# Performance work log

Hardware: AMD Instinct MI355X
Metric: run time of the kernel (lower is better)

Reference implementation:

```python
import jax, jax.numpy as jnp
import numpy as np

KERNEL_MUL = 2.0
KERNEL_NUM = 5


def setup_inputs() -> dict:
    key = jax.random.key(0)
    k1, k2 = jax.random.split(key)
    n, d = 4096, 256
    source = jax.random.normal(k1, (n, d), dtype=jnp.float32)
    target = jax.random.normal(k2, (n, d), dtype=jnp.float32) + 0.5  # slight domain shift
    return {"source": source, "target": target}


def _gaussian_kernel_sum(source, target):
    # total: (2n, d)
    total = jnp.concatenate([source, target], axis=0)
    n_samples = total.shape[0]
    # Pairwise squared L2 via x^2 + y^2 - 2xy (same math as the (2n,2n,d) broadcast)
    sq = jnp.sum(total * total, axis=1)  # (2n,)
    l2 = sq[:, None] + sq[None, :] - 2.0 * (total @ total.T)  # (2n, 2n)
    l2 = jnp.maximum(l2, 0.0)
    # bandwidth from detached distances (torch uses L2_distance.data)
    bandwidth = jax.lax.stop_gradient(jnp.sum(l2)) / (n_samples ** 2 - n_samples)
    bandwidth = bandwidth / (KERNEL_MUL ** (KERNEL_NUM // 2))
    # sum of multi-bandwidth RBF kernels
    kernels = jnp.zeros_like(l2)
    for i in range(KERNEL_NUM):
        kernels = kernels + jnp.exp(-l2 / (bandwidth * (KERNEL_MUL ** i)))
    return kernels


def reference(source, target):
    b = source.shape[0]
    kernels = _gaussian_kernel_sum(source, target)
    xx = jnp.mean(kernels[:b, :b])
    yy = jnp.mean(kernels[b:, b:])
    xy = jnp.mean(kernels[:b, b:])
    yx = jnp.mean(kernels[b:, :b])
    return xx + yy - xy - yx
```

## Files before the change

### kernel.cpp

```cpp
#include <hip/hip_runtime.h>

#define N_TOT 8192
#define NB    4096
#define DDIM  256
#define NTILE 64
#define NBLK  (NTILE * (NTILE + 1) / 2)

typedef __bf16 bf16x8 __attribute__((ext_vector_type(8)));
typedef float  f32x4  __attribute__((ext_vector_type(4)));

__device__ inline unsigned short f2bf_rne(float x) {
    unsigned int u = __float_as_uint(x);
    unsigned int r = (u + 0x7fffu + ((u >> 16) & 1u)) >> 16;
    return (unsigned short)r;
}

__device__ inline void gl2lds16(const unsigned short* g, unsigned short* l) {
    __builtin_amdgcn_global_load_lds(
        (const __attribute__((address_space(1))) unsigned int*)g,
        (__attribute__((address_space(3))) unsigned int*)l, 16, 0, 0);
}


__global__ void prep_rows(const float* __restrict__ src, const float* __restrict__ tgt,
                          float* __restrict__ sq, unsigned short* __restrict__ totb) {
    int wid  = threadIdx.x >> 6;
    int lane = threadIdx.x & 63;
    int row  = blockIdx.x * 4 + wid;
    const float* rp = (row < NB) ? (src + (size_t)row * DDIM)
                                 : (tgt + (size_t)(row - NB) * DDIM);
    float4 v = ((const float4*)rp)[lane];
    ushort4 o;
    o.x = f2bf_rne(v.x); o.y = f2bf_rne(v.y);
    o.z = f2bf_rne(v.z); o.w = f2bf_rne(v.w);
    ((ushort4*)(totb + (size_t)row * DDIM))[lane] = o;
    float s = v.x*v.x + v.y*v.y + v.z*v.z + v.w*v.w;
    #pragma unroll
    for (int off = 32; off > 0; off >>= 1) s += __shfl_down(s, off);
    if (lane == 0) sq[row] = s;
}

__global__ void col_sums(const float* __restrict__ src, const float* __restrict__ tgt,
                         float* __restrict__ wsf) {
    int d  = threadIdx.x;
    int r0 = blockIdx.x * 32;
    float local = 0.f;
    for (int r = 0; r < 32; ++r) {
        int row = r0 + r;
        const float* rp = (row < NB) ? (src + (size_t)row * DDIM)
                                     : (tgt + (size_t)(row - NB) * DDIM);
        local += rp[d];
    }
    atomicAdd(&wsf[64 + d], local);
}

__global__ void finalize_bw(float* __restrict__ wsf, const float* __restrict__ sq) {
    __shared__ float redA[4], redB[4];
    int t = threadIdx.x, lane = t & 63, w = t >> 6;
    float s1 = 0.f;
    for (int i = t; i < N_TOT; i += 256) s1 += sq[i];
    float sd = wsf[64 + t];
    float v2 = sd * sd;
    #pragma unroll
    for (int off = 32; off > 0; off >>= 1) {
        s1 += __shfl_down(s1, off);
        v2 += __shfl_down(v2, off);
    }
    if (lane == 0) { redA[w] = s1; redB[w] = v2; }
    __syncthreads();
    if (t == 0) {
        float S1   = redA[0] + redA[1] + redA[2] + redA[3];
        float sdot = redB[0] + redB[1] + redB[2] + redB[3];
        float bw_sum = 2.0f * (float)N_TOT * S1 - 2.0f * sdot;
        double denom = (double)N_TOT * (double)N_TOT - (double)N_TOT;
        float bandwidth = (float)((double)bw_sum / denom) * 0.25f;
        wsf[2] = 1.0f / bandwidth;
    }
}

__global__ __launch_bounds__(256) void mmd_tiles(const unsigned short* __restrict__ totb,
                                                 const float* __restrict__ sq,
                                                 const float* __restrict__ wsf,
                                                 float* __restrict__ part) {
    __shared__ unsigned short lds_a[128 * 32];
    __shared__ unsigned short lds_b[128 * 32];

    int idx = blockIdx.x;
    int ti = (int)((129.0f - sqrtf(16641.0f - 8.0f * (float)idx)) * 0.5f);
    if (ti > 63) ti = 63;
    if (ti < 0)  ti = 0;
    while ((ti * (129 - ti)) / 2 > idx) --ti;
    while (((ti + 1) * (128 - ti)) / 2 <= idx) ++ti;
    int tj = ti + idx - (ti * (129 - ti)) / 2;

    int t = threadIdx.x;
    int wid = t >> 6, lane = t & 63;
    int rl = lane & 15, q = lane >> 4;
    int gi0 = ti * 128, gj0 = tj * 128;
    int ia = (wid >> 1) * 64, jb = (wid & 1) * 64;

    const unsigned short* gA0 = totb + (size_t)(gi0 + (t >> 2)) * DDIM + (t & 3) * 8;
    const unsigned short* gA1 = gA0 + (size_t)64 * DDIM;
    const unsigned short* gB0 = totb + (size_t)(gj0 + (t >> 2)) * DDIM + (t & 3) * 8;
    const unsigned short* gB1 = gB0 + (size_t)64 * DDIM;
    unsigned short* lA0 = &lds_a[t * 8];
    unsigned short* lA1 = &lds_a[(t + 256) * 8];
    unsigned short* lB0 = &lds_b[t * 8];
    unsigned short* lB1 = &lds_b[(t + 256) * 8];

    f32x4 acc[4][4];
    #pragma unroll
    for (int m = 0; m < 4; ++m)
        #pragma unroll
        for (int n = 0; n < 4; ++n) acc[m][n] = (f32x4){0.f, 0.f, 0.f, 0.f};

    for (int k0 = 0; k0 < DDIM; k0 += 32) {
        gl2lds16(gA0 + k0, lA0);
        gl2lds16(gA1 + k0, lA1);
        gl2lds16(gB0 + k0, lB0);
        gl2lds16(gB1 + k0, lB1);
        __syncthreads();
        bf16x8 av[4], bv[4];
        #pragma unroll
        for (int m = 0; m < 4; ++m)
            av[m] = *(const bf16x8*)&lds_a[(ia + m * 16 + rl) * 32 + q * 8];
        #pragma unroll
        for (int n = 0; n < 4; ++n)
            bv[n] = *(const bf16x8*)&lds_b[(jb + n * 16 + rl) * 32 + q * 8];
        #pragma unroll
        for (int m = 0; m < 4; ++m)
            #pragma unroll
            for (int n = 0; n < 4; ++n)
                acc[m][n] = __builtin_amdgcn_mfma_f32_16x16x32_bf16(av[m], bv[n], acc[m][n], 0, 0, 0);
        __syncthreads();
    }

    float inv_bw16 = wsf[2] * 0.0625f;
    float local = 0.f;
    #pragma unroll
    for (int m = 0; m < 4; ++m) {
        f32x4 sqi = *(const f32x4*)(sq + gi0 + ia + m * 16 + q * 4);
        #pragma unroll
        for (int n = 0; n < 4; ++n) {
            float sqj = sq[gj0 + jb + n * 16 + rl];
            #pragma unroll
            for (int e = 0; e < 4; ++e) {
                float l2 = fmaxf(sqi[e] + sqj - 2.0f * acc[m][n][e], 0.0f);
                float e1 = __expf(-l2 * inv_bw16);
                float e2 = e1 * e1, e4 = e2 * e2, e8 = e4 * e4;
                local += e1 + e2 + e4 + e8 + e8 * e8;
            }
        }
    }
    #pragma unroll
    for (int off = 32; off > 0; off >>= 1) local += __shfl_down(local, off);
    float* red = (float*)lds_a;
    if (lane == 0) red[wid] = local;
    __syncthreads();
    if (t == 0) {
        float tot = red[0] + red[1] + red[2] + red[3];
        float scale = (((ti < 32) == (tj < 32)) ? 1.0f : -1.0f) * ((ti == tj) ? 1.0f : 2.0f);
        part[idx] = tot * scale;
    }
}

__global__ void write_out(const float* __restrict__ part, float* __restrict__ out) {
    __shared__ float red[4];
    int t = threadIdx.x, lane = t & 63, w = t >> 6;
    float s = 0.f;
    for (int i = t; i < NBLK; i += 256) s += part[i];
    #pragma unroll
    for (int off = 32; off > 0; off >>= 1) s += __shfl_down(s, off);
    if (lane == 0) red[w] = s;
    __syncthreads();
    if (t == 0)
        out[0] = (red[0] + red[1] + red[2] + red[3]) * (1.0f / ((float)NB * (float)NB));
}

extern "C" void kernel_launch(void* const* d_in, const int* in_sizes, int n_in,
                              void* d_out, int out_size, void* d_ws, size_t ws_size,
                              hipStream_t stream) {
    const float* src = (const float*)d_in[0];
    const float* tgt = (const float*)d_in[1];
    float* wsf  = (float*)d_ws;
    float* sq   = wsf + 512;
    float* part = wsf + 16384;
    unsigned short* totb = (unsigned short*)((char*)d_ws + 131072);

    hipMemsetAsync(d_ws, 0, 2048, stream);
    prep_rows<<<N_TOT / 4, 256, 0, stream>>>(src, tgt, sq, totb);
    col_sums<<<256, 256, 0, stream>>>(src, tgt, wsf);
    finalize_bw<<<1, 256, 0, stream>>>(wsf, sq);
    mmd_tiles<<<NBLK, 256, 0, stream>>>(totb, sq, wsf, part);
    write_out<<<1, 256, 0, stream>>>(part, (float*)d_out);
}
```

Before: 117.1 us.

## Fuse prep kernels, deepen K-tile, use exp2 epilogue, last-block final reduction

Merges the row conversion, squared-norm and column-sum kernels into one prep kernel that writes per-block column partials, so the memset and the atomics go away. The tile kernel now loads 64 K-elements per barrier pair, which halves the number of syncs. Its epilogue folds the bandwidth and log2(e) scale into one FMA plus a hardware exp2. The final write_out kernel is replaced by a last-block-done reduction using an atomic counter. Together these cut launch count and per-iteration sync overhead, at the cost of larger LDS use and a threadfence-based completion scheme.

```diff
diff --git a/kernel.cpp b/kernel.cpp
--- a/kernel.cpp
+++ b/kernel.cpp
@@ -5,6 +5,8 @@
 #define DDIM  256
 #define NTILE 64
 #define NBLK  (NTILE * (NTILE + 1) / 2)
+#define PREP_BLKS 256
+#define ROWS_PB   (N_TOT / PREP_BLKS)
 
 typedef __bf16 bf16x8 __attribute__((ext_vector_type(8)));
 typedef float  f32x4  __attribute__((ext_vector_type(4)));
@@ -22,45 +24,55 @@
 }
 
 
-__global__ void prep_rows(const float* __restrict__ src, const float* __restrict__ tgt,
-                          float* __restrict__ sq, unsigned short* __restrict__ totb) {
-    int wid  = threadIdx.x >> 6;
-    int lane = threadIdx.x & 63;
-    int row  = blockIdx.x * 4 + wid;
-    const float* rp = (row < NB) ? (src + (size_t)row * DDIM)
-                                 : (tgt + (size_t)(row - NB) * DDIM);
-    float4 v = ((const float4*)rp)[lane];
-    ushort4 o;
-    o.x = f2bf_rne(v.x); o.y = f2bf_rne(v.y);
-    o.z = f2bf_rne(v.z); o.w = f2bf_rne(v.w);
-    ((ushort4*)(totb + (size_t)row * DDIM))[lane] = o;
-    float s = v.x*v.x + v.y*v.y + v.z*v.z + v.w*v.w;
-    #pragma unroll
-    for (int off = 32; off > 0; off >>= 1) s += __shfl_down(s, off);
-    if (lane == 0) sq[row] = s;
-}
-
-__global__ void col_sums(const float* __restrict__ src, const float* __restrict__ tgt,
-                         float* __restrict__ wsf) {
-    int d  = threadIdx.x;
-    int r0 = blockIdx.x * 32;
-    float local = 0.f;
-    for (int r = 0; r < 32; ++r) {
-        int row = r0 + r;
+__global__ __launch_bounds__(256) void prep(const float* __restrict__ src,
+                                            const float* __restrict__ tgt,
+                                            float* __restrict__ sq,
+                                            unsigned short* __restrict__ totb,
+                                            float* __restrict__ colp) {
+    __shared__ float cs[4 * 256];
+    int t = threadIdx.x, w = t >> 6, lane = t & 63;
+    int row0 = blockIdx.x * ROWS_PB + w * (ROWS_PB / 4);
+    float4 csum = {0.f, 0.f, 0.f, 0.f};
+    #pragma unroll
+    for (int r = 0; r < ROWS_PB / 4; ++r) {
+        int row = row0 + r;
         const float* rp = (row < NB) ? (src + (size_t)row * DDIM)
                                      : (tgt + (size_t)(row - NB) * DDIM);
-        local += rp[d];
-    }
-    atomicAdd(&wsf[64 + d], local);
-}
-
-__global__ void finalize_bw(float* __restrict__ wsf, const float* __restrict__ sq) {
+        float4 v = ((const float4*)rp)[lane];
+        ushort4 o;
+        o.x = f2bf_rne(v.x); o.y = f2bf_rne(v.y);
+        o.z = f2bf_rne(v.z); o.w = f2bf_rne(v.w);
+        ((ushort4*)(totb + (size_t)row * DDIM))[lane] = o;
+        float s = v.x*v.x + v.y*v.y + v.z*v.z + v.w*v.w;
+        #pragma unroll
+        for (int off = 32; off > 0; off >>= 1) s += __shfl_down(s, off);
+        if (lane == 0) sq[row] = s;
+        csum.x += v.x; csum.y += v.y; csum.z += v.z; csum.w += v.w;
+    }
+    cs[w * 256 + lane * 4 + 0] = csum.x;
+    cs[w * 256 + lane * 4 + 1] = csum.y;
+    cs[w * 256 + lane * 4 + 2] = csum.z;
+    cs[w * 256 + lane * 4 + 3] = csum.w;
+    __syncthreads();
+    colp[blockIdx.x * 256 + t] = cs[t] + cs[256 + t] + cs[512 + t] + cs[768 + t];
+}
+
+__global__ void finalize_bw(const float* __restrict__ colp,
+                            const float* __restrict__ sq,
+                            float* __restrict__ wsf) {
     __shared__ float redA[4], redB[4];
     int t = threadIdx.x, lane = t & 63, w = t >> 6;
+    float sv0 = 0.f, sv1 = 0.f, sv2 = 0.f, sv3 = 0.f;
+    for (int b = 0; b < PREP_BLKS; b += 4) {
+        sv0 += colp[(b + 0) * 256 + t];
+        sv1 += colp[(b + 1) * 256 + t];
+        sv2 += colp[(b + 2) * 256 + t];
+        sv3 += colp[(b + 3) * 256 + t];
+    }
+    float sv = (sv0 + sv1) + (sv2 + sv3);
     float s1 = 0.f;
     for (int i = t; i < N_TOT; i += 256) s1 += sq[i];
-    float sd = wsf[64 + t];
-    float v2 = sd * sd;
+    float v2 = sv * sv;
     #pragma unroll
     for (int off = 32; off > 0; off >>= 1) {
         s1 += __shfl_down(s1, off);
@@ -74,16 +86,20 @@
         float bw_sum = 2.0f * (float)N_TOT * S1 - 2.0f * sdot;
         double denom = (double)N_TOT * (double)N_TOT - (double)N_TOT;
         float bandwidth = (float)((double)bw_sum / denom) * 0.25f;
-        wsf[2] = 1.0f / bandwidth;
+        wsf[2] = (1.0f / bandwidth) * 0.0625f * 1.44269504f;
+        ((unsigned int*)wsf)[3] = 0u;
     }
 }
 
 __global__ __launch_bounds__(256) void mmd_tiles(const unsigned short* __restrict__ totb,
                                                  const float* __restrict__ sq,
-                                                 const float* __restrict__ wsf,
-                                                 float* __restrict__ part) {
-    __shared__ unsigned short lds_a[128 * 32];
-    __shared__ unsigned short lds_b[128 * 32];
+                                                 float* __restrict__ wsf,
+                                                 float* __restrict__ part,
+                                                 float* __restrict__ out) {
+    __shared__ unsigned short lds_a[8192];
+    __shared__ unsigned short lds_b[8192];
+    __shared__ float redf[4];
+    __shared__ int amlast;
 
     int idx = blockIdx.x;
     int ti = (int)((129.0f - sqrtf(16641.0f - 8.0f * (float)idx)) * 0.5f);
@@ -99,14 +115,19 @@
     int gi0 = ti * 128, gj0 = tj * 128;
     int ia = (wid >> 1) * 64, jb = (wid & 1) * 64;
 
-    const unsigned short* gA0 = totb + (size_t)(gi0 + (t >> 2)) * DDIM + (t & 3) * 8;
-    const unsigned short* gA1 = gA0 + (size_t)64 * DDIM;
-    const unsigned short* gB0 = totb + (size_t)(gj0 + (t >> 2)) * DDIM + (t & 3) * 8;
-    const unsigned short* gB1 = gB0 + (size_t)64 * DDIM;
-    unsigned short* lA0 = &lds_a[t * 8];
-    unsigned short* lA1 = &lds_a[(t + 256) * 8];
-    unsigned short* lB0 = &lds_b[t * 8];
-    unsigned short* lB1 = &lds_b[(t + 256) * 8];
+    const unsigned short* gA[4]; const unsigned short* gB[4];
+    unsigned short* lA[4]; unsigned short* lB[4];
+    #pragma unroll
+    for (int i = 0; i < 4; ++i) {
+        int c = i * 256 + t;
+        int slab = c >> 9, rem = c & 511;
+        int row = rem >> 2, kg = rem & 3;
+        int col = slab * 32 + kg * 8;
+        gA[i] = totb + (size_t)(gi0 + row) * DDIM + col;
+        gB[i] = totb + (size_t)(gj0 + row) * DDIM + col;
+        lA[i] = &lds_a[c * 8];
+        lB[i] = &lds_b[c * 8];
+    }
 
     f32x4 acc[4][4];
     #pragma unroll
@@ -114,67 +135,75 @@
         #pragma unroll
         for (int n = 0; n < 4; ++n) acc[m][n] = (f32x4){0.f, 0.f, 0.f, 0.f};
 
-    for (int k0 = 0; k0 < DDIM; k0 += 32) {
-        gl2lds16(gA0 + k0, lA0);
-        gl2lds16(gA1 + k0, lA1);
-        gl2lds16(gB0 + k0, lB0);
-        gl2lds16(gB1 + k0, lB1);
+    for (int k0 = 0; k0 < DDIM; k0 += 64) {
+        #pragma unroll
+        for (int i = 0; i < 4; ++i) {
+            gl2lds16(gA[i] + k0, lA[i]);
+            gl2lds16(gB[i] + k0, lB[i]);
+        }
         __syncthreads();
-        bf16x8 av[4], bv[4];
-        #pragma unroll
-        for (int m = 0; m < 4; ++m)
-            av[m] = *(const bf16x8*)&lds_a[(ia + m * 16 + rl) * 32 + q * 8];
-        #pragma unroll
-        for (int n = 0; n < 4; ++n)
-            bv[n] = *(const bf16x8*)&lds_b[(jb + n * 16 + rl) * 32 + q * 8];
-        #pragma unroll
-        for (int m = 0; m < 4; ++m)
+        #pragma unroll
+        for (int h = 0; h < 2; ++h) {
+            bf16x8 av[4], bv[4];
+            #pragma unroll
+            for (int m = 0; m < 4; ++m)
+                av[m] = *(const bf16x8*)&lds_a[h * 4096 + (ia + m * 16 + rl) * 32 + q * 8];
             #pragma unroll
             for (int n = 0; n < 4; ++n)
-                acc[m][n] = __builtin_amdgcn_mfma_f32_16x16x32_bf16(av[m], bv[n], acc[m][n], 0, 0, 0);
+                bv[n] = *(const bf16x8*)&lds_b[h * 4096 + (jb + n * 16 + rl) * 32 + q * 8];
+            #pragma unroll
+            for (int m = 0; m < 4; ++m)
+                #pragma unroll
+                for (int n = 0; n < 4; ++n)
+                    acc[m][n] = __builtin_amdgcn_mfma_f32_16x16x32_bf16(av[m], bv[n], acc[m][n], 0, 0, 0);
+        }
         __syncthreads();
     }
 
-    float inv_bw16 = wsf[2] * 0.0625f;
+    float c  = wsf[2];
+    float tc = 2.0f * c;
     float local = 0.f;
     #pragma unroll
     for (int m = 0; m < 4; ++m) {
         f32x4 sqi = *(const f32x4*)(sq + gi0 + ia + m * 16 + q * 4);
+        f32x4 ai;
+        ai[0] = sqi[0] * c; ai[1] = sqi[1] * c; ai[2] = sqi[2] * c; ai[3] = sqi[3] * c;
         #pragma unroll
         for (int n = 0; n < 4; ++n) {
-            float sqj = sq[gj0 + jb + n * 16 + rl];
+            float bj = sq[gj0 + jb + n * 16 + rl] * c;
             #pragma unroll
             for (int e = 0; e < 4; ++e) {
-                float l2 = fmaxf(sqi[e] + sqj - 2.0f * acc[m][n][e], 0.0f);
-                float e1 = __expf(-l2 * inv_bw16);
+                float x  = __builtin_fmaf(acc[m][n][e], tc, -(ai[e] + bj));
+                float e1 = __builtin_amdgcn_exp2f(x);
                 float e2 = e1 * e1, e4 = e2 * e2, e8 = e4 * e4;
-                local += e1 + e2 + e4 + e8 + e8 * e8;
+                local += ((e1 + e2) + (e4 + e8)) + e8 * e8;
             }
         }
     }
     #pragma unroll
     for (int off = 32; off > 0; off >>= 1) local += __shfl_down(local, off);
-    float* red = (float*)lds_a;
-    if (lane == 0) red[wid] = local;
+    if (lane == 0) redf[wid] = local;
     __syncthreads();
     if (t == 0) {
-        float tot = red[0] + red[1] + red[2] + red[3];
+        float tot = redf[0] + redf[1] + redf[2] + redf[3];
         float scale = (((ti < 32) == (tj < 32)) ? 1.0f : -1.0f) * ((ti == tj) ? 1.0f : 2.0f);
         part[idx] = tot * scale;
-    }
-}
-
-__global__ void write_out(const float* __restrict__ part, float* __restrict__ out) {
-    __shared__ float red[4];
-    int t = threadIdx.x, lane = t & 63, w = t >> 6;
-    float s = 0.f;
-    for (int i = t; i < NBLK; i += 256) s += part[i];
-    #pragma unroll
-    for (int off = 32; off > 0; off >>= 1) s += __shfl_down(s, off);
-    if (lane == 0) red[w] = s;
-    __syncthreads();
-    if (t == 0)
-        out[0] = (red[0] + red[1] + red[2] + red[3]) * (1.0f / ((float)NB * (float)NB));
+        __threadfence();
+        unsigned int old = atomicAdd((unsigned int*)&wsf[3], 1u);
+        amlast = (old == NBLK - 1) ? 1 : 0;
+    }
+    __syncthreads();
+    if (amlast) {
+        __threadfence();
+        float s = 0.f;
+        for (int i = t; i < NBLK; i += 256) s += part[i];
+        #pragma unroll
+        for (int off = 32; off > 0; off >>= 1) s += __shfl_down(s, off);
+        if (lane == 0) redf[wid] = s;
+        __syncthreads();
+        if (t == 0)
+            out[0] = (redf[0] + redf[1] + redf[2] + redf[3]) * (1.0f / ((float)NB * (float)NB));
+    }
 }
 
 extern "C" void kernel_launch(void* const* d_in, const int* in_sizes, int n_in,
@@ -185,12 +214,10 @@
     float* wsf  = (float*)d_ws;
     float* sq   = wsf + 512;
     float* part = wsf + 16384;
-    unsigned short* totb = (unsigned short*)((char*)d_ws + 131072);
-
-    hipMemsetAsync(d_ws, 0, 2048, stream);
-    prep_rows<<<N_TOT / 4, 256, 0, stream>>>(src, tgt, sq, totb);
-    col_sums<<<256, 256, 0, stream>>>(src, tgt, wsf);
-    finalize_bw<<<1, 256, 0, stream>>>(wsf, sq);
-    mmd_tiles<<<NBLK, 256, 0, stream>>>(totb, sq, wsf, part);
-    write_out<<<1, 256, 0, stream>>>(part, (float*)d_out);
-}
+    float* colp = wsf + 32768;
+    unsigned short* totb = (unsigned short*)((char*)d_ws + 524288);
+
+    prep<<<PREP_BLKS, 256, 0, stream>>>(src, tgt, sq, totb, colp);
+    finalize_bw<<<1, 256, 0, stream>>>(colp, sq, wsf);
+    mmd_tiles<<<NBLK, 256, 0, stream>>>(totb, sq, wsf, part, (float*)d_out);
+}
```

New measurement: 143.4 us. 22.5% more time.
